# Kernel optimization log

Hardware: AMD Instinct MI355X
Metric: run time of the kernel (lower is better)

## Reference

```python
import jax, jax.numpy as jnp
import numpy as np

E = 100    # n_estimators
F = 10     # max_features
D = 100    # input feature dim
N = 8192   # batch
LAT = 2    # latent_dim
ENC_DIMS = [F, F // 2, F // 4, LAT]          # 10 -> 5 -> 2 -> 2
DEC_DIMS = [LAT, D // 4, D // 2, D]          # 2 -> 25 -> 50 -> 100


def _make_mlp(key, dims):
    ws, bs = [], []
    for i, (din, dout) in enumerate(zip(dims[:-1], dims[1:])):
        k = jax.random.fold_in(key, i)
        ws.append(jax.random.normal(k, (E, din, dout), dtype=jnp.float32) * 0.05)
        bs.append(jnp.zeros((E, dout), dtype=jnp.float32))
    return ws, bs


def setup_inputs() -> dict:
    key = jax.random.key(0)
    k_in, k_idx, k_enc, k_hi, k_lo = jax.random.split(key, 5)
    inputs = jax.random.normal(k_in, (N, D), dtype=jnp.float32)
    # per-estimator random feature subsets (original uses choice w/o replacement)
    randsamples = jax.random.randint(k_idx, (E, F), 0, D, dtype=jnp.int32)
    enc_ws, enc_bs = _make_mlp(k_enc, ENC_DIMS)
    hi_ws, hi_bs = _make_mlp(k_hi, DEC_DIMS)
    lo_ws, lo_bs = _make_mlp(k_lo, DEC_DIMS)
    d = {"inputs": inputs, "randsamples": randsamples}
    for i in range(3):
        d[f"enc_w{i}"], d[f"enc_b{i}"] = enc_ws[i], enc_bs[i]
        d[f"hi_w{i}"], d[f"hi_b{i}"] = hi_ws[i], hi_bs[i]
        d[f"lo_w{i}"], d[f"lo_b{i}"] = lo_ws[i], lo_bs[i]
    return d


def _mlp(x, ws, bs):
    # x: [E, N, din]; linear activation throughout (module default)
    for w, b in zip(ws, bs):
        x = jnp.einsum('enf,efg->eng', x, w) + b[:, None, :]
    return x


def reference(inputs, randsamples,
              enc_w0, enc_b0, enc_w1, enc_b1, enc_w2, enc_b2,
              hi_w0, hi_b0, hi_w1, hi_b1, hi_w2, hi_b2,
              lo_w0, lo_b0, lo_w1, lo_b1, lo_w2, lo_b2):
    # batched feature gather: [N, E, F] -> [E, N, F]
    xg = jnp.transpose(jnp.take(inputs, randsamples, axis=1), (1, 0, 2))
    z = _mlp(xg, [enc_w0, enc_w1, enc_w2], [enc_b0, enc_b1, enc_b2])   # [E, N, LAT]
    o_hi = _mlp(z, [hi_w0, hi_w1, hi_w2], [hi_b0, hi_b1, hi_b2])       # [E, N, D]
    o_lo = _mlp(z, [lo_w0, lo_w1, lo_w2], [lo_b0, lo_b1, lo_b2])       # [E, N, D]
    return (o_hi, o_lo)
```

## Files before the change

kernel.cpp:

```cpp
#include <hip/hip_runtime.h>

#define E_  100
#define F_  10
#define D_  100
#define N_  8192
#define TN  256
#define NTILES (N_ / TN)

typedef float f32x4 __attribute__((ext_vector_type(4)));

#define OFF_WHI  0
#define OFF_BHI  200
#define OFF_WLO  300
#define OFF_BLO  500
#define OFF_WENC 600
#define OFF_BENC 620
#define WS_PER_E 624

__global__ __launch_bounds__(128) void combine_kernel(
    const float* __restrict__ enc_w0, const float* __restrict__ enc_b0,
    const float* __restrict__ enc_w1, const float* __restrict__ enc_b1,
    const float* __restrict__ enc_w2, const float* __restrict__ enc_b2,
    const float* __restrict__ hi_w0,  const float* __restrict__ hi_b0,
    const float* __restrict__ hi_w1,  const float* __restrict__ hi_b1,
    const float* __restrict__ hi_w2,  const float* __restrict__ hi_b2,
    const float* __restrict__ lo_w0,  const float* __restrict__ lo_b0,
    const float* __restrict__ lo_w1,  const float* __restrict__ lo_b1,
    const float* __restrict__ lo_w2,  const float* __restrict__ lo_b2,
    float* __restrict__ ws)
{
    const int e = blockIdx.x;
    const int t = threadIdx.x;
    float* wsE = ws + (size_t)e * WS_PER_E;

    {
        const float* w0 = enc_w0 + e * 50;
        const float* w1 = enc_w1 + e * 10;
        const float* w2 = enc_w2 + e * 4;
        const float* b0 = enc_b0 + e * 5;
        const float* b1 = enc_b1 + e * 2;
        const float* b2 = enc_b2 + e * 2;

        __shared__ float sW01[20];
        __shared__ float sB01[2];
        if (t < 20) {
            int f = t >> 1, g = t & 1;
            float s = 0.f;
            for (int k = 0; k < 5; ++k) s += w0[f * 5 + k] * w1[k * 2 + g];
            sW01[t] = s;
        }
        if (t < 2) {
            float s = b1[t];
            for (int k = 0; k < 5; ++k) s += b0[k] * w1[k * 2 + t];
            sB01[t] = s;
        }
        __syncthreads();
        if (t < 20) {
            int f = t >> 1, g2 = t & 1;
            wsE[OFF_WENC + t] = sW01[f * 2 + 0] * w2[0 * 2 + g2]
                              + sW01[f * 2 + 1] * w2[1 * 2 + g2];
        }
        if (t < 2) {
            wsE[OFF_BENC + t] = sB01[0] * w2[0 * 2 + t] + sB01[1] * w2[1 * 2 + t] + b2[t];
        }
        __syncthreads();
    }

    __shared__ float sT[100];
    __shared__ float sU[50];
    for (int dec = 0; dec < 2; ++dec) {
        const float* w0 = (dec ? lo_w0 : hi_w0) + e * 50;
        const float* w1 = (dec ? lo_w1 : hi_w1) + e * 1250;
        const float* w2 = (dec ? lo_w2 : hi_w2) + e * 5000;
        const float* b0 = (dec ? lo_b0 : hi_b0) + e * 25;
        const float* b1 = (dec ? lo_b1 : hi_b1) + e * 50;
        const float* b2 = (dec ? lo_b2 : hi_b2) + e * 100;
        float* W = wsE + (dec ? OFF_WLO : OFF_WHI);
        float* B = wsE + (dec ? OFF_BLO : OFF_BHI);

        for (int i = t; i < 100; i += blockDim.x) {
            int a = i / 50, c = i % 50;
            float s = 0.f;
            for (int b = 0; b < 25; ++b) s += w0[a * 25 + b] * w1[b * 50 + c];
            sT[i] = s;
        }
        for (int i = t; i < 50; i += blockDim.x) {
            float s = b1[i];
            for (int b = 0; b < 25; ++b) s += b0[b] * w1[b * 50 + i];
            sU[i] = s;
        }
        __syncthreads();
        for (int i = t; i < 200; i += blockDim.x) {
            int a = i / 100, d = i % 100;
            float s = 0.f;
            for (int c = 0; c < 50; ++c) s += sT[a * 50 + c] * w2[c * 100 + d];
            W[i] = s;
        }
        for (int i = t; i < 100; i += blockDim.x) {
            float s = b2[i];
            for (int c = 0; c < 50; ++c) s += sU[c] * w2[c * 100 + i];
            B[i] = s;
        }
        __syncthreads();
    }
}

__global__ __launch_bounds__(256) void rancoders_main(
    const float* __restrict__ inputs,
    const int*   __restrict__ randsamples,
    const float* __restrict__ ws,
    float* __restrict__ out)
{
    const int e    = blockIdx.x >> 5;
    const int tile = blockIdx.x & (NTILES - 1);
    const int n0   = tile * TN;
    const int t    = threadIdx.x;

    __shared__ __align__(16) float sP[WS_PER_E];
    __shared__ int   sIdx[F_];
    __shared__ float sZ[TN * 2];

    const float* wsE = ws + (size_t)e * WS_PER_E;
    for (int i = t; i < 622; i += 256) sP[i] = wsE[i];
    if (t < F_) sIdx[t] = randsamples[e * F_ + t];
    __syncthreads();

    {
        const int n = n0 + t;
        const float* row = inputs + (size_t)n * D_;
        float z0 = sP[OFF_BENC + 0];
        float z1 = sP[OFF_BENC + 1];
#pragma unroll
        for (int f = 0; f < F_; ++f) {
            float v = row[sIdx[f]];
            z0 += v * sP[OFF_WENC + 2 * f + 0];
            z1 += v * sP[OFF_WENC + 2 * f + 1];
        }
        sZ[2 * t + 0] = z0;
        sZ[2 * t + 1] = z1;
    }
    __syncthreads();

    const int dq   = t & 31;
    const int rb   = t >> 5;
    const bool act = (dq < 25);
    const int d    = (act ? dq : 24) * 4;

    const f32x4 w0h = *(const f32x4*)&sP[OFF_WHI + d];
    const f32x4 w1h = *(const f32x4*)&sP[OFF_WHI + 100 + d];
    const f32x4 bh  = *(const f32x4*)&sP[OFF_BHI + d];
    const f32x4 w0l = *(const f32x4*)&sP[OFF_WLO + d];
    const f32x4 w1l = *(const f32x4*)&sP[OFF_WLO + 100 + d];
    const f32x4 bl  = *(const f32x4*)&sP[OFF_BLO + d];

    float* out_hi = out + (size_t)(e * N_ + n0) * D_;
    float* out_lo = out + (size_t)E_ * N_ * D_ + (size_t)(e * N_ + n0) * D_;

#pragma unroll 4
    for (int it = 0; it < TN / 8; ++it) {
        const int nl = it * 8 + rb;
        const float z0 = sZ[2 * nl + 0];
        const float z1 = sZ[2 * nl + 1];

        f32x4 oh = z0 * w0h + z1 * w1h + bh;
        f32x4 ol = z0 * w0l + z1 * w1l + bl;

        if (act) {
            const size_t off = (size_t)nl * D_ + (size_t)d;
            __builtin_nontemporal_store(oh, (f32x4*)&out_hi[off]);
            __builtin_nontemporal_store(ol, (f32x4*)&out_lo[off]);
        }
    }
}

extern "C" void kernel_launch(void* const* d_in, const int* in_sizes, int n_in,
                              void* d_out, int out_size, void* d_ws, size_t ws_size,
                              hipStream_t stream) {
    const float* inputs      = (const float*)d_in[0];
    const int*   randsamples = (const int*)d_in[1];
    const float* enc_w0 = (const float*)d_in[2];
    const float* enc_b0 = (const float*)d_in[3];
    const float* hi_w0  = (const float*)d_in[4];
    const float* hi_b0  = (const float*)d_in[5];
    const float* lo_w0  = (const float*)d_in[6];
    const float* lo_b0  = (const float*)d_in[7];
    const float* enc_w1 = (const float*)d_in[8];
    const float* enc_b1 = (const float*)d_in[9];
    const float* hi_w1  = (const float*)d_in[10];
    const float* hi_b1  = (const float*)d_in[11];
    const float* lo_w1  = (const float*)d_in[12];
    const float* lo_b1  = (const float*)d_in[13];
    const float* enc_w2 = (const float*)d_in[14];
    const float* enc_b2 = (const float*)d_in[15];
    const float* hi_w2  = (const float*)d_in[16];
    const float* hi_b2  = (const float*)d_in[17];
    const float* lo_w2  = (const float*)d_in[18];
    const float* lo_b2  = (const float*)d_in[19];

    float* ws  = (float*)d_ws;
    float* out = (float*)d_out;

    combine_kernel<<<E_, 128, 0, stream>>>(
        enc_w0, enc_b0, enc_w1, enc_b1, enc_w2, enc_b2,
        hi_w0, hi_b0, hi_w1, hi_b1, hi_w2, hi_b2,
        lo_w0, lo_b0, lo_w1, lo_b1, lo_w2, lo_b2, ws);

    rancoders_main<<<E_ * NTILES, 256, 0, stream>>>(inputs, randsamples, ws, out);
}
```

Before: 177.8 us.

## Transpose inputs to feature-major layout for coalesced gather; use plain stores

Adds a transpose of the input matrix into the workspace (fused into the weight-combine prep kernel as extra blocks) so the per-estimator feature gather reads contiguous columns instead of strided rows. Also switches output stores from nontemporal to ordinary stores and raises the unroll of the store loop. The layout path runs only when the workspace is large enough, and it costs an extra 3.2 MB read and write pass over the inputs. The main cost is the 655 MB output write, so the gather improvement may matter little.

```diff
diff --git a/kernel.cpp b/kernel.cpp
--- a/kernel.cpp
+++ b/kernel.cpp
@@ -16,8 +16,12 @@
 #define OFF_WENC 600
 #define OFF_BENC 620
 #define WS_PER_E 624
-
-__global__ __launch_bounds__(128) void combine_kernel(
+#define OFF_T    (E_ * WS_PER_E)
+#define WS_NEED_BYTES ((size_t)(OFF_T + D_ * N_) * 4)
+
+template <bool DO_TRANSPOSE>
+__global__ __launch_bounds__(128) void prep_kernel(
+    const float* __restrict__ inputs,
     const float* __restrict__ enc_w0, const float* __restrict__ enc_b0,
     const float* __restrict__ enc_w1, const float* __restrict__ enc_b1,
     const float* __restrict__ enc_w2, const float* __restrict__ enc_b2,
@@ -29,8 +33,19 @@
     const float* __restrict__ lo_w2,  const float* __restrict__ lo_b2,
     float* __restrict__ ws)
 {
+    const int t = threadIdx.x;
+
+    if (DO_TRANSPOSE && blockIdx.x >= E_) {
+        const int n0 = (blockIdx.x - E_) * 128;
+        float* T = ws + OFF_T;
+        const float* rowp = inputs + (size_t)(n0 + t) * D_;
+#pragma unroll 4
+        for (int d = 0; d < D_; ++d)
+            T[(size_t)d * N_ + n0 + t] = rowp[d];
+        return;
+    }
+
     const int e = blockIdx.x;
-    const int t = threadIdx.x;
     float* wsE = ws + (size_t)e * WS_PER_E;
 
     {
@@ -105,6 +120,7 @@
     }
 }
 
+template <bool USE_T>
 __global__ __launch_bounds__(256) void rancoders_main(
     const float* __restrict__ inputs,
     const int*   __restrict__ randsamples,
@@ -126,15 +142,24 @@
     __syncthreads();
 
     {
-        const int n = n0 + t;
-        const float* row = inputs + (size_t)n * D_;
         float z0 = sP[OFF_BENC + 0];
         float z1 = sP[OFF_BENC + 1];
+        if (USE_T) {
+            const float* T = ws + OFF_T;
 #pragma unroll
-        for (int f = 0; f < F_; ++f) {
-            float v = row[sIdx[f]];
-            z0 += v * sP[OFF_WENC + 2 * f + 0];
-            z1 += v * sP[OFF_WENC + 2 * f + 1];
+            for (int f = 0; f < F_; ++f) {
+                float v = T[(size_t)sIdx[f] * N_ + n0 + t];
+                z0 += v * sP[OFF_WENC + 2 * f + 0];
+                z1 += v * sP[OFF_WENC + 2 * f + 1];
+            }
+        } else {
+            const float* row = inputs + (size_t)(n0 + t) * D_;
+#pragma unroll
+            for (int f = 0; f < F_; ++f) {
+                float v = row[sIdx[f]];
+                z0 += v * sP[OFF_WENC + 2 * f + 0];
+                z1 += v * sP[OFF_WENC + 2 * f + 1];
+            }
         }
         sZ[2 * t + 0] = z0;
         sZ[2 * t + 1] = z1;
@@ -156,7 +181,7 @@
     float* out_hi = out + (size_t)(e * N_ + n0) * D_;
     float* out_lo = out + (size_t)E_ * N_ * D_ + (size_t)(e * N_ + n0) * D_;
 
-#pragma unroll 4
+#pragma unroll 8
     for (int it = 0; it < TN / 8; ++it) {
         const int nl = it * 8 + rb;
         const float z0 = sZ[2 * nl + 0];
@@ -167,8 +192,8 @@
 
         if (act) {
             const size_t off = (size_t)nl * D_ + (size_t)d;
-            __builtin_nontemporal_store(oh, (f32x4*)&out_hi[off]);
-            __builtin_nontemporal_store(ol, (f32x4*)&out_lo[off]);
+            *(f32x4*)&out_hi[off] = oh;
+            *(f32x4*)&out_lo[off] = ol;
         }
     }
 }
@@ -200,10 +225,23 @@
     float* ws  = (float*)d_ws;
     float* out = (float*)d_out;
 
-    combine_kernel<<<E_, 128, 0, stream>>>(
-        enc_w0, enc_b0, enc_w1, enc_b1, enc_w2, enc_b2,
-        hi_w0, hi_b0, hi_w1, hi_b1, hi_w2, hi_b2,
-        lo_w0, lo_b0, lo_w1, lo_b1, lo_w2, lo_b2, ws);
-
-    rancoders_main<<<E_ * NTILES, 256, 0, stream>>>(inputs, randsamples, ws, out);
+    const bool use_t = (ws_size >= WS_NEED_BYTES);
+
+    if (use_t) {
+        prep_kernel<true><<<E_ + N_ / 128, 128, 0, stream>>>(
+            inputs,
+            enc_w0, enc_b0, enc_w1, enc_b1, enc_w2, enc_b2,
+            hi_w0, hi_b0, hi_w1, hi_b1, hi_w2, hi_b2,
+            lo_w0, lo_b0, lo_w1, lo_b1, lo_w2, lo_b2, ws);
+        rancoders_main<true><<<E_ * NTILES, 256, 0, stream>>>(
+            inputs, randsamples, ws, out);
+    } else {
+        prep_kernel<false><<<E_, 128, 0, stream>>>(
+            inputs,
+            enc_w0, enc_b0, enc_w1, enc_b1, enc_w2, enc_b2,
+            hi_w0, hi_b0, hi_w1, hi_b1, hi_w2, hi_b2,
+            lo_w0, lo_b0, lo_w1, lo_b1, lo_w2, lo_b2, ws);
+        rancoders_main<false><<<E_ * NTILES, 256, 0, stream>>>(
+            inputs, randsamples, ws, out);
+    }
 }
```

After: 153.3 us. -13.8%, faster.

## Fuse weight-combine kernel into main kernel and restructure output store loop

Applied to the files above, without the earlier changes.

Removes the separate combine kernel and workspace; every block recomputes its estimator's collapsed affine weights (encoder and both decoders) in shared memory before producing outputs. This drops one kernel launch and the dependency between launches, at the cost of redundant per-block weight products (32 tiles per estimator each reading roughly 52 KB of decoder weights, mostly from cache). The store loop is also reorganised so each wave writes two rows per iteration, and nontemporal stores are replaced with regular stores.

```diff
diff --git a/kernel.cpp b/kernel.cpp
--- a/kernel.cpp
+++ b/kernel.cpp
@@ -9,15 +9,10 @@
 
 typedef float f32x4 __attribute__((ext_vector_type(4)));
 
-#define OFF_WHI  0
-#define OFF_BHI  200
-#define OFF_WLO  300
-#define OFF_BLO  500
-#define OFF_WENC 600
-#define OFF_BENC 620
-#define WS_PER_E 624
-
-__global__ __launch_bounds__(128) void combine_kernel(
+
+__global__ __launch_bounds__(256) void rancoders_fused(
+    const float* __restrict__ inputs,
+    const int*   __restrict__ randsamples,
     const float* __restrict__ enc_w0, const float* __restrict__ enc_b0,
     const float* __restrict__ enc_w1, const float* __restrict__ enc_b1,
     const float* __restrict__ enc_w2, const float* __restrict__ enc_b2,
@@ -27,88 +22,6 @@
     const float* __restrict__ lo_w0,  const float* __restrict__ lo_b0,
     const float* __restrict__ lo_w1,  const float* __restrict__ lo_b1,
     const float* __restrict__ lo_w2,  const float* __restrict__ lo_b2,
-    float* __restrict__ ws)
-{
-    const int e = blockIdx.x;
-    const int t = threadIdx.x;
-    float* wsE = ws + (size_t)e * WS_PER_E;
-
-    {
-        const float* w0 = enc_w0 + e * 50;
-        const float* w1 = enc_w1 + e * 10;
-        const float* w2 = enc_w2 + e * 4;
-        const float* b0 = enc_b0 + e * 5;
-        const float* b1 = enc_b1 + e * 2;
-        const float* b2 = enc_b2 + e * 2;
-
-        __shared__ float sW01[20];
-        __shared__ float sB01[2];
-        if (t < 20) {
-            int f = t >> 1, g = t & 1;
-            float s = 0.f;
-            for (int k = 0; k < 5; ++k) s += w0[f * 5 + k] * w1[k * 2 + g];
-            sW01[t] = s;
-        }
-        if (t < 2) {
-            float s = b1[t];
-            for (int k = 0; k < 5; ++k) s += b0[k] * w1[k * 2 + t];
-            sB01[t] = s;
-        }
-        __syncthreads();
-        if (t < 20) {
-            int f = t >> 1, g2 = t & 1;
-            wsE[OFF_WENC + t] = sW01[f * 2 + 0] * w2[0 * 2 + g2]
-                              + sW01[f * 2 + 1] * w2[1 * 2 + g2];
-        }
-        if (t < 2) {
-            wsE[OFF_BENC + t] = sB01[0] * w2[0 * 2 + t] + sB01[1] * w2[1 * 2 + t] + b2[t];
-        }
-        __syncthreads();
-    }
-
-    __shared__ float sT[100];
-    __shared__ float sU[50];
-    for (int dec = 0; dec < 2; ++dec) {
-        const float* w0 = (dec ? lo_w0 : hi_w0) + e * 50;
-        const float* w1 = (dec ? lo_w1 : hi_w1) + e * 1250;
-        const float* w2 = (dec ? lo_w2 : hi_w2) + e * 5000;
-        const float* b0 = (dec ? lo_b0 : hi_b0) + e * 25;
-        const float* b1 = (dec ? lo_b1 : hi_b1) + e * 50;
-        const float* b2 = (dec ? lo_b2 : hi_b2) + e * 100;
-        float* W = wsE + (dec ? OFF_WLO : OFF_WHI);
-        float* B = wsE + (dec ? OFF_BLO : OFF_BHI);
-
-        for (int i = t; i < 100; i += blockDim.x) {
-            int a = i / 50, c = i % 50;
-            float s = 0.f;
-            for (int b = 0; b < 25; ++b) s += w0[a * 25 + b] * w1[b * 50 + c];
-            sT[i] = s;
-        }
-        for (int i = t; i < 50; i += blockDim.x) {
-            float s = b1[i];
-            for (int b = 0; b < 25; ++b) s += b0[b] * w1[b * 50 + i];
-            sU[i] = s;
-        }
-        __syncthreads();
-        for (int i = t; i < 200; i += blockDim.x) {
-            int a = i / 100, d = i % 100;
-            float s = 0.f;
-            for (int c = 0; c < 50; ++c) s += sT[a * 50 + c] * w2[c * 100 + d];
-            W[i] = s;
-        }
-        for (int i = t; i < 100; i += blockDim.x) {
-            float s = b2[i];
-            for (int c = 0; c < 50; ++c) s += sU[c] * w2[c * 100 + i];
-            B[i] = s;
-        }
-        __syncthreads();
-    }
-}
-
-__global__ __launch_bounds__(256) void rancoders_main(
-    const float* __restrict__ inputs,
-    const int*   __restrict__ randsamples,
-    const float* __restrict__ ws,
     float* __restrict__ out)
 {
     const int e    = blockIdx.x >> 5;
@@ -116,59 +29,151 @@
     const int n0   = tile * TN;
     const int t    = threadIdx.x;
 
-    __shared__ __align__(16) float sP[WS_PER_E];
-    __shared__ int   sIdx[F_];
-    __shared__ float sZ[TN * 2];
-
-    const float* wsE = ws + (size_t)e * WS_PER_E;
-    for (int i = t; i < 622; i += 256) sP[i] = wsE[i];
+    __shared__ __align__(16) float sP[624];
+    __shared__ float  sW01[20];
+    __shared__ float  sB01[2];
+    __shared__ float  sTU[300];
+    __shared__ int    sIdx[F_];
+    __shared__ float2 sZ2[TN];
+
     if (t < F_) sIdx[t] = randsamples[e * F_ + t];
+
+    const float* ew0 = enc_w0 + e * 50;
+    const float* ew1 = enc_w1 + e * 10;
+    const float* ew2 = enc_w2 + e * 4;
+
+    for (int i = t; i < 322; i += 256) {
+        if (i < 100) {
+            const int a = i / 50, c = i % 50;
+            const float* w0 = hi_w0 + e * 50;
+            const float* w1 = hi_w1 + e * 1250;
+            float s = 0.f;
+            for (int b = 0; b < 25; ++b) s += w0[a * 25 + b] * w1[b * 50 + c];
+            sTU[i] = s;
+        } else if (i < 150) {
+            const int c = i - 100;
+            const float* w1 = hi_w1 + e * 1250;
+            const float* b0 = hi_b0 + e * 25;
+            float s = hi_b1[e * 50 + c];
+            for (int b = 0; b < 25; ++b) s += b0[b] * w1[b * 50 + c];
+            sTU[i] = s;
+        } else if (i < 250) {
+            const int j = i - 150;
+            const int a = j / 50, c = j % 50;
+            const float* w0 = lo_w0 + e * 50;
+            const float* w1 = lo_w1 + e * 1250;
+            float s = 0.f;
+            for (int b = 0; b < 25; ++b) s += w0[a * 25 + b] * w1[b * 50 + c];
+            sTU[i] = s;
+        } else if (i < 300) {
+            const int c = i - 250;
+            const float* w1 = lo_w1 + e * 1250;
+            const float* b0 = lo_b0 + e * 25;
+            float s = lo_b1[e * 50 + c];
+            for (int b = 0; b < 25; ++b) s += b0[b] * w1[b * 50 + c];
+            sTU[i] = s;
+        } else if (i < 320) {
+            const int j = i - 300;
+            const int f = j >> 1, g = j & 1;
+            float s = 0.f;
+            for (int k = 0; k < 5; ++k) s += ew0[f * 5 + k] * ew1[k * 2 + g];
+            sW01[j] = s;
+        } else {
+            const int g = i - 320;
+            float s = enc_b1[e * 2 + g];
+            for (int k = 0; k < 5; ++k) s += enc_b0[e * 5 + k] * ew1[k * 2 + g];
+            sB01[g] = s;
+        }
+    }
     __syncthreads();
 
+    for (int i = t; i < 622; i += 256) {
+        if (i < 200) {
+            const int a = i / 100, d = i % 100;
+            const float* w2 = hi_w2 + e * 5000;
+            float s = 0.f;
+            for (int c = 0; c < 50; ++c) s += sTU[a * 50 + c] * w2[c * 100 + d];
+            sP[i] = s;
+        } else if (i < 300) {
+            const int d = i - 200;
+            const float* w2 = hi_w2 + e * 5000;
+            float s = hi_b2[e * 100 + d];
+            for (int c = 0; c < 50; ++c) s += sTU[100 + c] * w2[c * 100 + d];
+            sP[i] = s;
+        } else if (i < 500) {
+            const int j = i - 300;
+            const int a = j / 100, d = j % 100;
+            const float* w2 = lo_w2 + e * 5000;
+            float s = 0.f;
+            for (int c = 0; c < 50; ++c) s += sTU[150 + a * 50 + c] * w2[c * 100 + d];
+            sP[i] = s;
+        } else if (i < 600) {
+            const int d = i - 500;
+            const float* w2 = lo_w2 + e * 5000;
+            float s = lo_b2[e * 100 + d];
+            for (int c = 0; c < 50; ++c) s += sTU[250 + c] * w2[c * 100 + d];
+            sP[i] = s;
+        } else if (i < 620) {
+            const int j = i - 600;
+            const int f = j >> 1, g = j & 1;
+            sP[i] = sW01[f * 2 + 0] * ew2[0 * 2 + g]
+                  + sW01[f * 2 + 1] * ew2[1 * 2 + g];
+        } else {
+            const int g = i - 620;
+            sP[i] = sB01[0] * ew2[0 * 2 + g] + sB01[1] * ew2[1 * 2 + g]
+                  + enc_b2[e * 2 + g];
+        }
+    }
+    __syncthreads();
+
     {
-        const int n = n0 + t;
-        const float* row = inputs + (size_t)n * D_;
-        float z0 = sP[OFF_BENC + 0];
-        float z1 = sP[OFF_BENC + 1];
+        const float* row = inputs + (size_t)(n0 + t) * D_;
+        float z0 = sP[620];
+        float z1 = sP[621];
 #pragma unroll
         for (int f = 0; f < F_; ++f) {
-            float v = row[sIdx[f]];
-            z0 += v * sP[OFF_WENC + 2 * f + 0];
-            z1 += v * sP[OFF_WENC + 2 * f + 1];
-        }
-        sZ[2 * t + 0] = z0;
-        sZ[2 * t + 1] = z1;
+            const float v = row[sIdx[f]];
+            z0 += v * sP[600 + 2 * f + 0];
+            z1 += v * sP[600 + 2 * f + 1];
+        }
+        sZ2[t] = make_float2(z0, z1);
     }
     __syncthreads();
 
-    const int dq   = t & 31;
-    const int rb   = t >> 5;
+    const int w    = t >> 6;
+    const int l    = t & 63;
+    const int h    = l >> 5;
+    const int dq   = l & 31;
     const bool act = (dq < 25);
     const int d    = (act ? dq : 24) * 4;
 
-    const f32x4 w0h = *(const f32x4*)&sP[OFF_WHI + d];
-    const f32x4 w1h = *(const f32x4*)&sP[OFF_WHI + 100 + d];
-    const f32x4 bh  = *(const f32x4*)&sP[OFF_BHI + d];
-    const f32x4 w0l = *(const f32x4*)&sP[OFF_WLO + d];
-    const f32x4 w1l = *(const f32x4*)&sP[OFF_WLO + 100 + d];
-    const f32x4 bl  = *(const f32x4*)&sP[OFF_BLO + d];
+    const f32x4 w0h = *(const f32x4*)&sP[0 + d];
+    const f32x4 w1h = *(const f32x4*)&sP[100 + d];
+    const f32x4 bh  = *(const f32x4*)&sP[200 + d];
+    const f32x4 w0l = *(const f32x4*)&sP[300 + d];
+    const f32x4 w1l = *(const f32x4*)&sP[400 + d];
+    const f32x4 bl  = *(const f32x4*)&sP[500 + d];
 
     float* out_hi = out + (size_t)(e * N_ + n0) * D_;
     float* out_lo = out + (size_t)E_ * N_ * D_ + (size_t)(e * N_ + n0) * D_;
 
-#pragma unroll 4
-    for (int it = 0; it < TN / 8; ++it) {
-        const int nl = it * 8 + rb;
-        const float z0 = sZ[2 * nl + 0];
-        const float z1 = sZ[2 * nl + 1];
-
-        f32x4 oh = z0 * w0h + z1 * w1h + bh;
-        f32x4 ol = z0 * w0l + z1 * w1l + bl;
+#pragma unroll 8
+    for (int it = 0; it < TN / 16; ++it) {
+        const int r0 = it * 16 + w * 4 + h;
+        const float2 za = sZ2[r0];
+        const float2 zb = sZ2[r0 + 2];
+
+        f32x4 oha = za.x * w0h + za.y * w1h + bh;
+        f32x4 ohb = zb.x * w0h + zb.y * w1h + bh;
+        f32x4 ola = za.x * w0l + za.y * w1l + bl;
+        f32x4 olb = zb.x * w0l + zb.y * w1l + bl;
 
         if (act) {
-            const size_t off = (size_t)nl * D_ + (size_t)d;
-            __builtin_nontemporal_store(oh, (f32x4*)&out_hi[off]);
-            __builtin_nontemporal_store(ol, (f32x4*)&out_lo[off]);
+            const size_t off = (size_t)r0 * D_ + (size_t)d;
+            *(f32x4*)&out_hi[off]          = oha;
+            *(f32x4*)&out_hi[off + 2 * D_] = ohb;
+            *(f32x4*)&out_lo[off]          = ola;
+            *(f32x4*)&out_lo[off + 2 * D_] = olb;
         }
     }
 }
@@ -197,13 +202,12 @@
     const float* lo_w2  = (const float*)d_in[18];
     const float* lo_b2  = (const float*)d_in[19];
 
-    float* ws  = (float*)d_ws;
     float* out = (float*)d_out;
-
-    combine_kernel<<<E_, 128, 0, stream>>>(
+    (void)d_ws; (void)ws_size;
+
+    rancoders_fused<<<E_ * NTILES, 256, 0, stream>>>(
+        inputs, randsamples,
         enc_w0, enc_b0, enc_w1, enc_b1, enc_w2, enc_b2,
         hi_w0, hi_b0, hi_w1, hi_b1, hi_w2, hi_b2,
-        lo_w0, lo_b0, lo_w1, lo_b1, lo_w2, lo_b2, ws);
-
-    rancoders_main<<<E_ * NTILES, 256, 0, stream>>>(inputs, randsamples, ws, out);
+        lo_w0, lo_b0, lo_w1, lo_b1, lo_w2, lo_b2, out);
 }
```

Result: slower. 274.5 us (+54.4%).
